# Optimization experiments

Hardware: AMD Instinct MI355X
Metric: run time of the kernel (lower is better)

The kernel has to match this reference:

```python
import jax, jax.numpy as jnp
import numpy as np


def _lstm_step(h, c, x, W_ih, W_hh, b_ih, b_hh):
    # PyTorch gate order: i, f, g, o
    gates = x @ W_ih.T + b_ih + h @ W_hh.T + b_hh
    i, f, g, o = jnp.split(gates, 4, axis=-1)
    c = jax.nn.sigmoid(f) * c + jax.nn.sigmoid(i) * jnp.tanh(g)
    h = jax.nn.sigmoid(o) * jnp.tanh(c)
    return h, c


def setup_inputs() -> dict:
    key = jax.random.key(0)
    ks = jax.random.split(key, 12)
    B, T = 256, 256
    S, A, H, K = 64, 16, 512, 512
    D = S + A  # 80
    s = 1.0 / np.sqrt(H)
    u = lambda k, shape, sc: jax.random.uniform(k, shape, jnp.float32, -sc, sc)
    return {
        "traj": jax.random.normal(ks[0], (B, T, D), jnp.float32),
        "seq_len": T,
        "enc_W_ih": u(ks[1], (4 * H, D), s),
        "enc_W_hh": u(ks[2], (4 * H, H), s),
        "enc_b_ih": u(ks[3], (4 * H,), s),
        "enc_b_hh": u(ks[4], (4 * H,), s),
        "embeddings": jax.random.uniform(ks[5], (K, H), jnp.float32, -1.0 / K, 1.0 / K),
        "dec_W_ih": u(ks[6], (4 * H, D), s),
        "dec_W_hh": u(ks[7], (4 * H, H), s),
        "dec_b_ih": u(ks[8], (4 * H,), s),
        "dec_b_hh": u(ks[9], (4 * H,), s),
        "fc_W": u(ks[10], (D, H), s),
        "fc_b": u(ks[11], (D,), s),
    }


def reference(traj, seq_len, enc_W_ih, enc_W_hh, enc_b_ih, enc_b_hh,
              embeddings, dec_W_ih, dec_W_hh, dec_b_ih, dec_b_hh, fc_W, fc_b):
    B = traj.shape[0]
    H = enc_W_hh.shape[1]
    D = traj.shape[-1]

    # ---- Encoder: many-to-one LSTM, keep final hidden state ----
    def enc_step(carry, x_t):
        h, c = carry
        h, c = _lstm_step(h, c, x_t, enc_W_ih, enc_W_hh, enc_b_ih, enc_b_hh)
        return (h, c), None
    h0 = jnp.zeros((B, H), traj.dtype)
    (z, _), _ = jax.lax.scan(enc_step, (h0, h0), jnp.swapaxes(traj, 0, 1))

    # ---- Vector quantizer ----
    d = (jnp.sum(z * z, axis=1, keepdims=True)
         + jnp.sum(embeddings * embeddings, axis=1)
         - 2.0 * z @ embeddings.T)  # [B, K]
    idx = jnp.argmin(d, axis=1)
    quantized = embeddings[idx]  # [B, H]
    e_latent = jnp.mean((jax.lax.stop_gradient(quantized) - z) ** 2)
    q_latent = jnp.mean((quantized - jax.lax.stop_gradient(z)) ** 2)
    vq_loss = q_latent + 0.25 * e_latent

    def dec_step(carry, _):
        h, c, x = carry
        h, c = _lstm_step(h, c, x, dec_W_ih, dec_W_hh, dec_b_ih, dec_b_hh)
        y = h @ fc_W.T + fc_b
        return (h, c, y), y
    x0 = jnp.zeros((B, D), traj.dtype)
    c0 = jnp.zeros((B, H), traj.dtype)
    _, ys = jax.lax.scan(dec_step, (quantized, c0, x0), None, length=seq_len)
    recon = jnp.swapaxes(ys, 0, 1)  # [B, seq_len, D]
    return recon, vq_loss, idx[:, None]
```

## Files before the change

kernel.cpp:

```cpp
#include <hip/hip_runtime.h>
#include <math.h>

#define BB 256
#define TT 256
#define DDIM 80
#define HDIM 512
#define ROWSTRIDE 20480

#define WS_HA    0
#define WS_CD    131072
#define WS_BAR   262144
#define WS_HB    263168
#define WS_QUANT 394240
#define WS_VQP   525312
#define WS_BENC  525568
#define WS_BDEC0 527616
#define WS_BEFF  529664
#define WS_WEFF  531712

typedef _Float16 f16;
typedef f16 half4_t __attribute__((ext_vector_type(4)));
typedef f16 half8_t __attribute__((ext_vector_type(8)));
typedef float float4_t __attribute__((ext_vector_type(4)));

__device__ __forceinline__ float sigmoidf_(float v) { return 1.0f / (1.0f + expf(-v)); }

__device__ __forceinline__ void llc_store_f32(float* p, float v) {
  asm volatile("global_store_dword %0, %1, off sc0 sc1" :: "v"(p), "v"(v) : "memory");
}
__device__ __forceinline__ void llc_store_i32(int* p, int v) {
  asm volatile("global_store_dword %0, %1, off sc0 sc1" :: "v"(p), "v"(v) : "memory");
}
__device__ __forceinline__ int llc_load_i32(const int* p) {
  int v;
  asm volatile("global_load_dword %0, %1, off sc0 sc1\n\ts_waitcnt vmcnt(0)"
               : "=v"(v) : "v"(p) : "memory");
  return v;
}
__device__ __forceinline__ void wait_vm0() {
  asm volatile("s_waitcnt vmcnt(0)" ::: "memory");
}
__device__ __forceinline__ void llc_load_4xf4(
    const float4* p0, const float4* p1, const float4* p2, const float4* p3,
    float4& a0, float4& a1, float4& a2, float4& a3) {
  asm volatile(
      "global_load_dwordx4 %0, %4, off sc0 sc1\n\t"
      "global_load_dwordx4 %1, %5, off sc0 sc1\n\t"
      "global_load_dwordx4 %2, %6, off sc0 sc1\n\t"
      "global_load_dwordx4 %3, %7, off sc0 sc1\n\t"
      "s_waitcnt vmcnt(0)"
      : "=&v"(a0), "=&v"(a1), "=&v"(a2), "=&v"(a3)
      : "v"(p0), "v"(p1), "v"(p2), "v"(p3)
      : "memory");
}

__global__ __launch_bounds__(256) void zero_kernel(float4* __restrict__ p, int n4) {
  int i = blockIdx.x * 256 + threadIdx.x;
  if (i < n4) p[i] = make_float4(0.f, 0.f, 0.f, 0.f);
}

__global__ __launch_bounds__(256) void bias_init_kernel(
    const float* __restrict__ eb1, const float* __restrict__ eb2,
    const float* __restrict__ db1, const float* __restrict__ db2,
    const float* __restrict__ dWih, const float* __restrict__ fcb,
    float* __restrict__ b_enc, float* __restrict__ b_dec0,
    float* __restrict__ b_eff) {
  int n = blockIdx.x * 256 + threadIdx.x;
  b_enc[n] = eb1[n] + eb2[n];
  float bd = db1[n] + db2[n];
  b_dec0[n] = bd;
  float acc = bd;
  #pragma unroll 16
  for (int d = 0; d < DDIM; d++) acc += dWih[n * DDIM + d] * fcb[d];
  b_eff[n] = acc;
}

__global__ __launch_bounds__(256) void fold_kernel(
    const float* __restrict__ dWih, const float* __restrict__ dWhh,
    const float* __restrict__ fcW, float* __restrict__ W_eff) {
  int n = blockIdx.x;
  int tid = threadIdx.x;
  __shared__ float sw[DDIM];
  if (tid < DDIM) sw[tid] = dWih[n * DDIM + tid];
  __syncthreads();
  for (int k = tid; k < HDIM; k += 256) {
    float acc = dWhh[n * HDIM + k];
    #pragma unroll 16
    for (int d = 0; d < DDIM; d++) acc += sw[d] * fcW[d * HDIM + k];
    W_eff[n * HDIM + k] = acc;
  }
}

__global__ __launch_bounds__(256) void lstm_step_kernel(
    const float* __restrict__ Whh, const float* __restrict__ bias,
    const float* __restrict__ h_in, float* __restrict__ c,
    float* __restrict__ h_out) {
  __shared__ float sh[16][516];
  int tid = threadIdx.x;
  int rt = blockIdx.x & 15, jt = blockIdx.x >> 4;
  int row0 = rt << 4;
  for (int i = tid; i < 2048; i += 256) {
    int r = i >> 7, kq = i & 127;
    float4 v = *(const float4*)(h_in + (size_t)(row0 + r) * HDIM + (kq << 2));
    *(float4*)&sh[r][kq << 2] = v;
  }
  __syncthreads();
  int r = tid & 15, j0 = tid >> 4;
  int j = (jt << 4) + j0;
  float a0 = bias[j], a1 = bias[512 + j], a2 = bias[1024 + j], a3 = bias[1536 + j];
  const float4* w0 = (const float4*)(Whh + (size_t)j * HDIM);
  const float4* w1 = (const float4*)(Whh + (size_t)(512 + j) * HDIM);
  const float4* w2 = (const float4*)(Whh + (size_t)(1024 + j) * HDIM);
  const float4* w3 = (const float4*)(Whh + (size_t)(1536 + j) * HDIM);
  const float4* hv = (const float4*)&sh[r][0];
  #pragma unroll 4
  for (int kq = 0; kq < 128; kq++) {
    float4 h4 = hv[kq];
    float4 q0 = w0[kq], q1 = w1[kq], q2 = w2[kq], q3 = w3[kq];
    a0 += h4.x * q0.x + h4.y * q0.y + h4.z * q0.z + h4.w * q0.w;
    a1 += h4.x * q1.x + h4.y * q1.y + h4.z * q1.z + h4.w * q1.w;
    a2 += h4.x * q2.x + h4.y * q2.y + h4.z * q2.z + h4.w * q2.w;
    a3 += h4.x * q3.x + h4.y * q3.y + h4.z * q3.z + h4.w * q3.w;
  }
  size_t idx = (size_t)(row0 + r) * HDIM + j;
  float cv = c[idx];
  float cn = sigmoidf_(a1) * cv + sigmoidf_(a0) * tanhf(a2);
  float hn = sigmoidf_(a3) * tanhf(cn);
  c[idx] = cn;
  h_out[idx] = hn;
}

template <int IS_DEC>
__global__ __launch_bounds__(512, 2) void lstm_persist(
    const float* __restrict__ W,
    const float* __restrict__ Wih,
    const float* __restrict__ bias,
    const float* __restrict__ traj,
    const float* __restrict__ c_init,
    const float* __restrict__ fcW, const float* __restrict__ fcb,
    float* __restrict__ recon,
    float* __restrict__ hA, float* __restrict__ hB,
    int* __restrict__ flags) {
  constexpr int KT  = IS_DEC ? 16 : 19;
  constexpr int AST = IS_DEC ? 520 : 616;
  constexpr int RST = 132;
  __shared__ f16 Ahi[16 * AST];
  __shared__ f16 Alo[16 * AST];
  __shared__ float red[16 * RST];
  __shared__ float ypart[IS_DEC ? 8 * 260 : 4];

  const int tid = threadIdx.x;
  const int bid = blockIdx.x;
  const int rt = bid & 15, jt = bid >> 4;
  const int r0 = rt * 16, d0 = jt * 32;
  const int wv = __builtin_amdgcn_readfirstlane(tid >> 6);
  const int l15 = tid & 15;
  const int q = (tid >> 4) & 3;
  const int dh = wv >> 2, nt = wv & 3;

  #define SPLITW(vv, it) { \
    int i = tid + (it) * 512; \
    int off = (i >> 7) * AST + (i & 127) * 4; \
    half4_t hi4, lo4; \
    float f0 = vv.x, f1 = vv.y, f2 = vv.z, f3 = vv.w; \
    f16 a = (f16)f0, b = (f16)f1, cc = (f16)f2, d = (f16)f3; \
    hi4[0] = a; hi4[1] = b; hi4[2] = cc; hi4[3] = d; \
    lo4[0] = (f16)(f0 - (float)a); lo4[1] = (f16)(f1 - (float)b); \
    lo4[2] = (f16)(f2 - (float)cc); lo4[3] = (f16)(f3 - (float)d); \
    *(half4_t*)&Ahi[off] = hi4; *(half4_t*)&Alo[off] = lo4; }

  const int grow = nt * 512 + d0 + dh * 16 + l15;
  half8_t Whi[KT], Wlo[KT];
  #pragma unroll
  for (int kt = 0; kt < KT; kt++) {
    #pragma unroll
    for (int j = 0; j < 8; j++) {
      int k = kt * 32 + q * 8 + j;
      float w;
      if (k < 512) w = W[(size_t)grow * HDIM + k];
      else {
        int kx = k - 512;
        w = (!IS_DEC && kx < DDIM) ? Wih[(size_t)grow * DDIM + kx] : 0.f;
      }
      f16 hi = (f16)w;
      Whi[kt][j] = hi;
      Wlo[kt][j] = (f16)(w - (float)hi);
    }
  }
  const float breg = bias[grow];

  half8_t Fhi[2], Flo[2];
  float ybias = 0.f;
  if (IS_DEC && jt < 5) {
    const int drow = jt * 16 + l15;
    #pragma unroll
    for (int kk = 0; kk < 2; kk++) {
      const int kt = wv * 2 + kk;
      #pragma unroll
      for (int j = 0; j < 8; j++) {
        float w = fcW[(size_t)drow * HDIM + kt * 32 + q * 8 + j];
        f16 hi = (f16)w;
        Fhi[kk][j] = hi;
        Flo[kk][j] = (f16)(w - (float)hi);
      }
    }
    ybias = fcb[jt * 16 + l15];
  }

  const int eb = tid >> 5, ed = tid & 31;
  float c_reg = IS_DEC ? c_init[(size_t)(r0 + eb) * HDIM + d0 + ed] : 0.f;
  __syncthreads();

  const int t_begin = IS_DEC ? 1 : 0;
  for (int t = t_begin; t < TT; t++) {
    const float* hin = (t & 1) ? hB : hA;
    float* hout = (t & 1) ? hA : hB;

    float4 xv0;
    if (!IS_DEC && tid < 384) {
      int row = tid / 24, c4 = tid % 24;
      xv0 = (c4 < 20)
          ? *(const float4*)(traj + (size_t)(r0 + row) * ROWSTRIDE +
                             (size_t)t * DDIM + c4 * 4)
          : make_float4(0.f, 0.f, 0.f, 0.f);
    }

    {
      const float4* gp = (const float4*)(hin + (size_t)r0 * HDIM);
      float4 v0, v1, v2, v3;
      llc_load_4xf4(gp + tid + 0 * 512, gp + tid + 1 * 512,
                    gp + tid + 2 * 512, gp + tid + 3 * 512,
                    v0, v1, v2, v3);
      SPLITW(v0, 0); SPLITW(v1, 1); SPLITW(v2, 2); SPLITW(v3, 3);
    }
    if (!IS_DEC && tid < 384) {
      int row = tid / 24, c4 = tid % 24;
      int off = row * AST + 512 + c4 * 4;
      half4_t hi4, lo4;
      float f0 = xv0.x, f1 = xv0.y, f2 = xv0.z, f3 = xv0.w;
      f16 a = (f16)f0, b = (f16)f1, cc = (f16)f2, d = (f16)f3;
      hi4[0] = a; hi4[1] = b; hi4[2] = cc; hi4[3] = d;
      lo4[0] = (f16)(f0 - (float)a); lo4[1] = (f16)(f1 - (float)b);
      lo4[2] = (f16)(f2 - (float)cc); lo4[3] = (f16)(f3 - (float)d);
      *(half4_t*)&Ahi[off] = hi4; *(half4_t*)&Alo[off] = lo4;
    }
    __syncthreads();

    {
      float4_t acc0 = {breg, breg, breg, breg};
      float4_t acc1 = {0.f, 0.f, 0.f, 0.f};
      const int abase = l15 * AST + q * 8;
      #pragma unroll
      for (int kt = 0; kt < KT; kt++) {
        half8_t ahi = *(const half8_t*)&Ahi[abase + kt * 32];
        half8_t alo = *(const half8_t*)&Alo[abase + kt * 32];
        if (kt & 1) {
          acc1 = __builtin_amdgcn_mfma_f32_16x16x32_f16(ahi, Whi[kt], acc1, 0, 0, 0);
          acc1 = __builtin_amdgcn_mfma_f32_16x16x32_f16(alo, Whi[kt], acc1, 0, 0, 0);
          acc1 = __builtin_amdgcn_mfma_f32_16x16x32_f16(ahi, Wlo[kt], acc1, 0, 0, 0);
          acc1 = __builtin_amdgcn_mfma_f32_16x16x32_f16(alo, Wlo[kt], acc1, 0, 0, 0);
        } else {
          acc0 = __builtin_amdgcn_mfma_f32_16x16x32_f16(ahi, Whi[kt], acc0, 0, 0, 0);
          acc0 = __builtin_amdgcn_mfma_f32_16x16x32_f16(alo, Whi[kt], acc0, 0, 0, 0);
          acc0 = __builtin_amdgcn_mfma_f32_16x16x32_f16(ahi, Wlo[kt], acc0, 0, 0, 0);
          acc0 = __builtin_amdgcn_mfma_f32_16x16x32_f16(alo, Wlo[kt], acc0, 0, 0, 0);
        }
      }
      float4_t C = acc0 + acc1;
      #pragma unroll
      for (int i = 0; i < 4; i++)
        red[(q * 4 + i) * RST + nt * 32 + dh * 16 + l15] = C[i];
    }
    __syncthreads();

    {
      float ig = red[eb * RST + ed];
      float fg = red[eb * RST + 32 + ed];
      float gg = red[eb * RST + 64 + ed];
      float og = red[eb * RST + 96 + ed];
      float cn = sigmoidf_(fg) * c_reg + sigmoidf_(ig) * tanhf(gg);
      c_reg = cn;
      llc_store_f32(&hout[(size_t)(r0 + eb) * HDIM + d0 + ed],
                    sigmoidf_(og) * tanhf(cn));
    }
    wait_vm0();
    __syncthreads();

    const int done = t - t_begin + 1;
    const bool do_bar = IS_DEC || t < TT - 1;
    if (do_bar && tid == 0) llc_store_i32(&flags[rt * 16 + jt], done);

    if (IS_DEC && jt < 5) {
      float4_t ya = {0.f, 0.f, 0.f, 0.f};
      #pragma unroll
      for (int kk = 0; kk < 2; kk++) {
        const int kt = wv * 2 + kk;
        const int ao = l15 * AST + kt * 32 + q * 8;
        half8_t ahi = *(const half8_t*)&Ahi[ao];
        half8_t alo = *(const half8_t*)&Alo[ao];
        ya = __builtin_amdgcn_mfma_f32_16x16x32_f16(ahi, Fhi[kk], ya, 0, 0, 0);
        ya = __builtin_amdgcn_mfma_f32_16x16x32_f16(alo, Fhi[kk], ya, 0, 0, 0);
        ya = __builtin_amdgcn_mfma_f32_16x16x32_f16(ahi, Flo[kk], ya, 0, 0, 0);
        ya = __builtin_amdgcn_mfma_f32_16x16x32_f16(alo, Flo[kk], ya, 0, 0, 0);
      }
      #pragma unroll
      for (int i = 0; i < 4; i++)
        ypart[wv * 260 + (q * 4 + i) * 16 + l15] = ya[i];
    }
    if (IS_DEC) __syncthreads();
    if (IS_DEC && jt < 5 && tid < 256) {
      float acc = ybias;
      #pragma unroll
      for (int w8 = 0; w8 < 8; w8++) acc += ypart[w8 * 260 + tid];
      recon[(size_t)(r0 + (tid >> 4)) * ROWSTRIDE + (size_t)(t - 1) * DDIM +
            jt * 16 + (tid & 15)] = acc;
    }

    if (do_bar) {
      if (tid < 64) {
        const int* fp = flags + rt * 16 + (tid & 15);
        while (llc_load_i32(fp) < done) __builtin_amdgcn_s_sleep(1);
      }
      __syncthreads();
    }
  }

  if (IS_DEC) {
    if (jt >= 5) return;
    {
      const float4* gp = (const float4*)(hA + (size_t)r0 * HDIM);
      float4 v0, v1, v2, v3;
      llc_load_4xf4(gp + tid + 0 * 512, gp + tid + 1 * 512,
                    gp + tid + 2 * 512, gp + tid + 3 * 512,
                    v0, v1, v2, v3);
      SPLITW(v0, 0); SPLITW(v1, 1); SPLITW(v2, 2); SPLITW(v3, 3);
    }
    __syncthreads();
    {
      float4_t ya = {0.f, 0.f, 0.f, 0.f};
      #pragma unroll
      for (int kk = 0; kk < 2; kk++) {
        const int kt = wv * 2 + kk;
        const int ao = l15 * AST + kt * 32 + q * 8;
        half8_t ahi = *(const half8_t*)&Ahi[ao];
        half8_t alo = *(const half8_t*)&Alo[ao];
        ya = __builtin_amdgcn_mfma_f32_16x16x32_f16(ahi, Fhi[kk], ya, 0, 0, 0);
        ya = __builtin_amdgcn_mfma_f32_16x16x32_f16(alo, Fhi[kk], ya, 0, 0, 0);
        ya = __builtin_amdgcn_mfma_f32_16x16x32_f16(ahi, Flo[kk], ya, 0, 0, 0);
        ya = __builtin_amdgcn_mfma_f32_16x16x32_f16(alo, Flo[kk], ya, 0, 0, 0);
      }
      #pragma unroll
      for (int i = 0; i < 4; i++)
        ypart[wv * 260 + (q * 4 + i) * 16 + l15] = ya[i];
    }
    __syncthreads();
    if (tid < 256) {
      float acc = ybias;
      #pragma unroll
      for (int w8 = 0; w8 < 8; w8++) acc += ypart[w8 * 260 + tid];
      recon[(size_t)(r0 + (tid >> 4)) * ROWSTRIDE + (size_t)255 * DDIM +
            jt * 16 + (tid & 15)] = acc;
    }
  }
  #undef SPLITW
}

__global__ __launch_bounds__(256) void vq_kernel(
    const float* __restrict__ z, const float* __restrict__ emb,
    float* __restrict__ quant, float* __restrict__ vq_part,
    float* __restrict__ out_idx) {
  __shared__ float sz[512];
  __shared__ float sd[256];
  __shared__ int si[256];
  int b = blockIdx.x, tid = threadIdx.x;
  sz[tid] = z[(size_t)b * HDIM + tid];
  sz[tid + 256] = z[(size_t)b * HDIM + 256 + tid];
  __syncthreads();
  float bd = 3.4e38f;
  int bk = 0;
  for (int k = tid; k < 512; k += 256) {
    const float4* e4 = (const float4*)(emb + (size_t)k * HDIM);
    const float4* z4 = (const float4*)sz;
    float dot = 0.f, ee = 0.f;
    #pragma unroll 4
    for (int qq = 0; qq < 128; qq++) {
      float4 ev = e4[qq], zv = z4[qq];
      dot += ev.x * zv.x + ev.y * zv.y + ev.z * zv.z + ev.w * zv.w;
      ee += ev.x * ev.x + ev.y * ev.y + ev.z * ev.z + ev.w * ev.w;
    }
    float dist = ee - 2.f * dot;
    if (dist < bd) { bd = dist; bk = k; }
  }
  sd[tid] = bd; si[tid] = bk;
  __syncthreads();
  for (int s = 128; s > 0; s >>= 1) {
    if (tid < s) {
      float od = sd[tid + s]; int ok = si[tid + s];
      if (od < sd[tid] || (od == sd[tid] && ok < si[tid])) { sd[tid] = od; si[tid] = ok; }
    }
    __syncthreads();
  }
  int kbest = si[0];
  __syncthreads();
  float e0 = emb[(size_t)kbest * HDIM + tid];
  float e1 = emb[(size_t)kbest * HDIM + 256 + tid];
  quant[(size_t)b * HDIM + tid] = e0;
  quant[(size_t)b * HDIM + 256 + tid] = e1;
  float q0 = e0 - sz[tid], q1 = e1 - sz[tid + 256];
  sd[tid] = q0 * q0 + q1 * q1;
  __syncthreads();
  for (int st = 128; st > 0; st >>= 1) {
    if (tid < st) sd[tid] += sd[tid + st];
    __syncthreads();
  }
  if (tid == 0) { vq_part[b] = sd[0]; out_idx[b] = (float)kbest; }
}

__global__ __launch_bounds__(256) void vq_reduce_kernel(const float* __restrict__ vq_part,
                                                        float* __restrict__ out_loss) {
  __shared__ float s[256];
  int tid = threadIdx.x;
  s[tid] = vq_part[tid];
  __syncthreads();
  for (int st = 128; st > 0; st >>= 1) {
    if (tid < st) s[tid] += s[tid + st];
    __syncthreads();
  }
  if (tid == 0) out_loss[0] = s[0] * 1.25f / (float)(BB * HDIM);
}

extern "C" void kernel_launch(void* const* d_in, const int* in_sizes, int n_in,
                              void* d_out, int out_size, void* d_ws, size_t ws_size,
                              hipStream_t stream) {
  const float* traj = (const float*)d_in[0];
  const float* eWih = (const float*)d_in[2];
  const float* eWhh = (const float*)d_in[3];
  const float* eb1  = (const float*)d_in[4];
  const float* eb2  = (const float*)d_in[5];
  const float* emb  = (const float*)d_in[6];
  const float* dWih = (const float*)d_in[7];
  const float* dWhh = (const float*)d_in[8];
  const float* db1  = (const float*)d_in[9];
  const float* db2  = (const float*)d_in[10];
  const float* fcW  = (const float*)d_in[11];
  const float* fcb  = (const float*)d_in[12];

  float* out = (float*)d_out;
  float* recon = out;
  float* out_loss = out + 5242880;
  float* out_idx = out + 5242881;

  float* ws = (float*)d_ws;
  float* hA      = ws + WS_HA;
  float* cD      = ws + WS_CD;
  int*   bar     = (int*)(ws + WS_BAR);
  float* hB      = ws + WS_HB;
  float* quant   = ws + WS_QUANT;
  float* vq_part = ws + WS_VQP;
  float* b_enc   = ws + WS_BENC;
  float* b_dec0  = ws + WS_BDEC0;
  float* b_eff   = ws + WS_BEFF;
  float* W_eff   = ws + WS_WEFF;

  zero_kernel<<<257, 256, 0, stream>>>((float4*)ws, 65792);
  bias_init_kernel<<<8, 256, 0, stream>>>(eb1, eb2, db1, db2, dWih, fcb,
                                          b_enc, b_dec0, b_eff);
  fold_kernel<<<2048, 256, 0, stream>>>(dWih, dWhh, fcW, W_eff);

  lstm_persist<0><<<256, 512, 0, stream>>>(
      eWhh, eWih, b_enc, traj, nullptr, nullptr, nullptr, nullptr, hA, hB, bar);

  vq_kernel<<<256, 256, 0, stream>>>(hA, emb, quant, vq_part, out_idx);
  vq_reduce_kernel<<<1, 256, 0, stream>>>(vq_part, out_loss);

  lstm_step_kernel<<<512, 256, 0, stream>>>(dWhh, b_dec0, quant, cD, hB);
  lstm_persist<1><<<256, 512, 0, stream>>>(
      W_eff, nullptr, b_eff, nullptr, cD, fcW, fcb, recon, hA, hB, bar + 256);
}
```

Measured before the change: 2.134 ms.

## Overlap hidden-state load with MFMA by splitting K range per step

Each timestep's hidden-state load is rearranged so every thread loads column chunks. The first half is converted and synced, MFMAs on K tiles 0-7 run while the second half is still in flight, and the second half is finished before the remaining tiles. At t=0 in the encoder the global load is replaced by zero-filling shared memory, and the flag spin loop drops its s_sleep to cut barrier wake-up latency. The change adds an extra __syncthreads per step and raises spin pressure on the flag cache lines.

```diff
diff --git a/kernel.cpp b/kernel.cpp
--- a/kernel.cpp
+++ b/kernel.cpp
@@ -40,8 +40,8 @@
 __device__ __forceinline__ void wait_vm0() {
   asm volatile("s_waitcnt vmcnt(0)" ::: "memory");
 }
-__device__ __forceinline__ void llc_load_4xf4(
-    const float4* p0, const float4* p1, const float4* p2, const float4* p3,
+__device__ __forceinline__ void llc_load_4xf4_cols(
+    const float4* base,
     float4& a0, float4& a1, float4& a2, float4& a3) {
   asm volatile(
       "global_load_dwordx4 %0, %4, off sc0 sc1\n\t"
@@ -50,7 +50,7 @@
       "global_load_dwordx4 %3, %7, off sc0 sc1\n\t"
       "s_waitcnt vmcnt(0)"
       : "=&v"(a0), "=&v"(a1), "=&v"(a2), "=&v"(a3)
-      : "v"(p0), "v"(p1), "v"(p2), "v"(p3)
+      : "v"(base), "v"(base + 32), "v"(base + 64), "v"(base + 96)
       : "memory");
 }
 
@@ -158,9 +158,8 @@
   const int q = (tid >> 4) & 3;
   const int dh = wv >> 2, nt = wv & 3;
 
-  #define SPLITW(vv, it) { \
-    int i = tid + (it) * 512; \
-    int off = (i >> 7) * AST + (i & 127) * 4; \
+  #define SPLITC(vv, k) { \
+    int off = (tid >> 5) * AST + (((tid & 31) + (k) * 32) << 2); \
     half4_t hi4, lo4; \
     float f0 = vv.x, f1 = vv.y, f2 = vv.z, f3 = vv.w; \
     f16 a = (f16)f0, b = (f16)f1, cc = (f16)f2, d = (f16)f3; \
@@ -211,6 +210,24 @@
   float c_reg = IS_DEC ? c_init[(size_t)(r0 + eb) * HDIM + d0 + ed] : 0.f;
   __syncthreads();
 
+  #define MFMA_RANGE(LO, HI) { \
+    _Pragma("unroll") \
+    for (int kt = (LO); kt < (HI); kt++) { \
+      half8_t ahi = *(const half8_t*)&Ahi[abase + kt * 32]; \
+      half8_t alo = *(const half8_t*)&Alo[abase + kt * 32]; \
+      if (kt & 1) { \
+        acc1 = __builtin_amdgcn_mfma_f32_16x16x32_f16(ahi, Whi[kt], acc1, 0, 0, 0); \
+        acc1 = __builtin_amdgcn_mfma_f32_16x16x32_f16(alo, Whi[kt], acc1, 0, 0, 0); \
+        acc1 = __builtin_amdgcn_mfma_f32_16x16x32_f16(ahi, Wlo[kt], acc1, 0, 0, 0); \
+        acc1 = __builtin_amdgcn_mfma_f32_16x16x32_f16(alo, Wlo[kt], acc1, 0, 0, 0); \
+      } else { \
+        acc0 = __builtin_amdgcn_mfma_f32_16x16x32_f16(ahi, Whi[kt], acc0, 0, 0, 0); \
+        acc0 = __builtin_amdgcn_mfma_f32_16x16x32_f16(alo, Whi[kt], acc0, 0, 0, 0); \
+        acc0 = __builtin_amdgcn_mfma_f32_16x16x32_f16(ahi, Wlo[kt], acc0, 0, 0, 0); \
+        acc0 = __builtin_amdgcn_mfma_f32_16x16x32_f16(alo, Wlo[kt], acc0, 0, 0, 0); \
+      } \
+    } }
+
   const int t_begin = IS_DEC ? 1 : 0;
   for (int t = t_begin; t < TT; t++) {
     const float* hin = (t & 1) ? hB : hA;
@@ -225,13 +242,39 @@
           : make_float4(0.f, 0.f, 0.f, 0.f);
     }
 
-    {
-      const float4* gp = (const float4*)(hin + (size_t)r0 * HDIM);
-      float4 v0, v1, v2, v3;
-      llc_load_4xf4(gp + tid + 0 * 512, gp + tid + 1 * 512,
-                    gp + tid + 2 * 512, gp + tid + 3 * 512,
-                    v0, v1, v2, v3);
-      SPLITW(v0, 0); SPLITW(v1, 1); SPLITW(v2, 2); SPLITW(v3, 3);
+    float4 v0, v1, v2, v3;
+    const float4* base =
+        (const float4*)(hin + (size_t)r0 * HDIM) + (tid >> 5) * 128 + (tid & 31);
+    const bool is_t0 = (!IS_DEC && t == 0);
+    if (!is_t0) {
+      asm volatile(
+          "global_load_dwordx4 %0, %4, off sc0 sc1\n\t"
+          "global_load_dwordx4 %1, %5, off sc0 sc1\n\t"
+          "global_load_dwordx4 %2, %6, off sc0 sc1\n\t"
+          "global_load_dwordx4 %3, %7, off sc0 sc1"
+          : "=&v"(v0), "=&v"(v1), "=&v"(v2), "=&v"(v3)
+          : "v"(base), "v"(base + 32), "v"(base + 64), "v"(base + 96)
+          : "memory");
+      asm volatile("s_waitcnt vmcnt(2)" ::: "memory");
+      __builtin_amdgcn_sched_barrier(0);
+      SPLITC(v0, 0); SPLITC(v1, 1);
+    } else {
+      const int fo = (tid >> 5) * AST + ((tid & 31) << 4);
+      uint4 z4; z4.x = 0; z4.y = 0; z4.z = 0; z4.w = 0;
+      *(uint4*)&Ahi[fo] = z4; *(uint4*)&Ahi[fo + 8] = z4;
+      *(uint4*)&Alo[fo] = z4; *(uint4*)&Alo[fo + 8] = z4;
+    }
+    __syncthreads();
+
+    float4_t acc0 = {breg, breg, breg, breg};
+    float4_t acc1 = {0.f, 0.f, 0.f, 0.f};
+    const int abase = l15 * AST + q * 8;
+    MFMA_RANGE(0, 8);
+
+    if (!is_t0) {
+      asm volatile("s_waitcnt vmcnt(0)" ::: "memory");
+      __builtin_amdgcn_sched_barrier(0);
+      SPLITC(v2, 2); SPLITC(v3, 3);
     }
     if (!IS_DEC && tid < 384) {
       int row = tid / 24, c4 = tid % 24;
@@ -245,27 +288,8 @@
       *(half4_t*)&Ahi[off] = hi4; *(half4_t*)&Alo[off] = lo4;
     }
     __syncthreads();
-
+    MFMA_RANGE(8, KT);
     {
-      float4_t acc0 = {breg, breg, breg, breg};
-      float4_t acc1 = {0.f, 0.f, 0.f, 0.f};
-      const int abase = l15 * AST + q * 8;
-      #pragma unroll
-      for (int kt = 0; kt < KT; kt++) {
-        half8_t ahi = *(const half8_t*)&Ahi[abase + kt * 32];
-        half8_t alo = *(const half8_t*)&Alo[abase + kt * 32];
-        if (kt & 1) {
-          acc1 = __builtin_amdgcn_mfma_f32_16x16x32_f16(ahi, Whi[kt], acc1, 0, 0, 0);
-          acc1 = __builtin_amdgcn_mfma_f32_16x16x32_f16(alo, Whi[kt], acc1, 0, 0, 0);
-          acc1 = __builtin_amdgcn_mfma_f32_16x16x32_f16(ahi, Wlo[kt], acc1, 0, 0, 0);
-          acc1 = __builtin_amdgcn_mfma_f32_16x16x32_f16(alo, Wlo[kt], acc1, 0, 0, 0);
-        } else {
-          acc0 = __builtin_amdgcn_mfma_f32_16x16x32_f16(ahi, Whi[kt], acc0, 0, 0, 0);
-          acc0 = __builtin_amdgcn_mfma_f32_16x16x32_f16(alo, Whi[kt], acc0, 0, 0, 0);
-          acc0 = __builtin_amdgcn_mfma_f32_16x16x32_f16(ahi, Wlo[kt], acc0, 0, 0, 0);
-          acc0 = __builtin_amdgcn_mfma_f32_16x16x32_f16(alo, Wlo[kt], acc0, 0, 0, 0);
-        }
-      }
       float4_t C = acc0 + acc1;
       #pragma unroll
       for (int i = 0; i < 4; i++)
@@ -319,7 +343,7 @@
     if (do_bar) {
       if (tid < 64) {
         const int* fp = flags + rt * 16 + (tid & 15);
-        while (llc_load_i32(fp) < done) __builtin_amdgcn_s_sleep(1);
+        while (llc_load_i32(fp) < done) {}
       }
       __syncthreads();
     }
@@ -328,12 +352,11 @@
   if (IS_DEC) {
     if (jt >= 5) return;
     {
-      const float4* gp = (const float4*)(hA + (size_t)r0 * HDIM);
+      const float4* base =
+          (const float4*)(hA + (size_t)r0 * HDIM) + (tid >> 5) * 128 + (tid & 31);
       float4 v0, v1, v2, v3;
-      llc_load_4xf4(gp + tid + 0 * 512, gp + tid + 1 * 512,
-                    gp + tid + 2 * 512, gp + tid + 3 * 512,
-                    v0, v1, v2, v3);
-      SPLITW(v0, 0); SPLITW(v1, 1); SPLITW(v2, 2); SPLITW(v3, 3);
+      llc_load_4xf4_cols(base, v0, v1, v2, v3);
+      SPLITC(v0, 0); SPLITC(v1, 1); SPLITC(v2, 2); SPLITC(v3, 3);
     }
     __syncthreads();
     {
@@ -362,7 +385,8 @@
             jt * 16 + (tid & 15)] = acc;
     }
   }
-  #undef SPLITW
+  #undef SPLITC
+  #undef MFMA_RANGE
 }
 
 __global__ __launch_bounds__(256) void vq_kernel(
```

Result: no change. 2.131 ms (-0.2%).
